# Optimization experiments

Measured on AMD Instinct MI355X. Metric: run time of the kernel, lower is better.

The kernel has to match this reference:

```python
import jax, jax.numpy as jnp
import numpy as np
import math

B, L, D, H = 2, 2048, 1024, 16
DK = D // H


def setup_inputs() -> dict:
    key = jax.random.key(0)
    ks = jax.random.split(key, 11)
    s = 1.0 / math.sqrt(D)
    inp = {
        "query": jax.random.normal(ks[0], (B, L, D), jnp.float32),
        "key": jax.random.normal(ks[1], (B, L, D), jnp.float32),
        "value": jax.random.normal(ks[2], (B, L, D), jnp.float32),
        # mask == True (==1) means masked-out; causal mask over future positions
        "mask": jnp.triu(jnp.ones((L, L), dtype=bool), k=1),
        "Wq": jax.random.normal(ks[3], (D, D), jnp.float32) * s,
        "bq": jnp.zeros((D,), jnp.float32),
        "Wk": jax.random.normal(ks[4], (D, D), jnp.float32) * s,
        "bk": jnp.zeros((D,), jnp.float32),
        "Wv": jax.random.normal(ks[5], (D, D), jnp.float32) * s,
        "bv": jnp.zeros((D,), jnp.float32),
        "Wo": jax.random.normal(ks[6], (D, D), jnp.float32) * s,
        "bo": jnp.zeros((D,), jnp.float32),
    }
    return inp


def reference(query, key, value, mask, Wq, bq, Wk, bk, Wv, bv, Wo, bo):
    # Linear projections, then split heads: [B, L, D] -> [B, H, L, DK]
    def proj(x, W, b):
        return (x @ W.T + b).reshape(B, -1, H, DK).transpose(0, 2, 1, 3)

    Q = proj(query, Wq, bq)
    K = proj(key, Wk, bk)
    V = proj(value, Wv, bv)

    scale = 1.0 / math.sqrt(DK)
    scores = jnp.einsum("bhqd,bhkd->bhqk", Q, K) * scale  # [B,H,Lq,Lk]
    scores = jnp.where(mask, -jnp.inf, scores)
    attn = jax.nn.softmax(scores, axis=-1)  # dropout p=0 (eval mode)
    out = jnp.einsum("bhqk,bhkd->bhqd", attn, V)
    out = out.transpose(0, 2, 1, 3).reshape(B, -1, D)  # merge heads
    return out @ Wo.T + bo
```

## Files before the change

### kernel.cpp

```cpp
#include <hip/hip_runtime.h>
#include <hip/hip_bf16.h>
#include <math.h>

#define NL 2048
#define ND 1024

typedef __attribute__((ext_vector_type(8))) __bf16 bf16x8;
typedef __attribute__((ext_vector_type(4))) float f32x4;
typedef __attribute__((ext_vector_type(16))) float f32x16;
typedef __attribute__((ext_vector_type(4))) short short4v;
typedef __attribute__((ext_vector_type(2))) unsigned uint2v;
typedef __attribute__((ext_vector_type(4))) unsigned uint4v;

__device__ __forceinline__ short f2bf(float f) {
    union { float f; unsigned u; } v; v.f = f;
    unsigned u = v.u;
    u += 0x7FFF + ((u >> 16) & 1);
    return (short)(u >> 16);
}

__device__ __forceinline__ unsigned cvtpk2(float lo, float hi) {
    unsigned r;
    asm("v_cvt_pk_bf16_f32 %0, %1, %2" : "=v"(r) : "v"(lo), "v"(hi));
    return r;
}

__device__ __forceinline__ void gload16(const short* g, short* l) {
    __builtin_amdgcn_global_load_lds(
        (const __attribute__((address_space(1))) void*)g,
        (__attribute__((address_space(3))) void*)l, 16, 0, 0);
}

__global__ __launch_bounds__(256) void cvt_f32_bf16_3(const float* __restrict__ a,
                                                      const float* __restrict__ b,
                                                      const float* __restrict__ c,
                                                      short* __restrict__ dst, int per) {
    const float* src = blockIdx.y == 0 ? a : blockIdx.y == 1 ? b : c;
    short* d = dst + (size_t)blockIdx.y * per;
    int i = (blockIdx.x * 256 + threadIdx.x) * 8;
    if (i < per) {
        f32x4 v0 = *(const f32x4*)&src[i];
        f32x4 v1 = *(const f32x4*)&src[i + 4];
        uint4v u = { cvtpk2(v0[0], v0[1]), cvtpk2(v0[2], v0[3]),
                     cvtpk2(v1[0], v1[1]), cvtpk2(v1[2], v1[3]) };
        *(uint4v*)&d[i] = u;
    }
}

__global__ __launch_bounds__(256) void gemm_qkv(
    const float* __restrict__ Xq, const float* __restrict__ Xk, const float* __restrict__ Xv,
    const short* __restrict__ Wqb, const short* __restrict__ Wkb, const short* __restrict__ Wvb,
    const float* __restrict__ bq, const float* __restrict__ bk, const float* __restrict__ bv,
    short* __restrict__ oq, short* __restrict__ ok, short* __restrict__ ov) {
    __shared__ alignas(16) short As[128 * 40];
    __shared__ alignas(16) short Bs[128 * 32];

    const int bid  = blockIdx.x;
    const int xcd  = bid & 7, slot = bid >> 3;
    const int panel = xcd * 12 + (slot >> 3);
    const int z    = panel >> 5;
    const int m0   = (panel & 31) * 128;
    const int n0   = (slot & 7) * 128;

    const float* X  = z == 0 ? Xq : z == 1 ? Xk : Xv;
    const short* Wb = z == 0 ? Wqb : z == 1 ? Wkb : Wvb;
    const float* bi = z == 0 ? bq : z == 1 ? bk : bv;
    short* outp     = z == 0 ? oq : z == 1 ? ok : ov;
    const float scl = z == 0 ? 0.125f * 1.44269504088896f : 1.0f;

    const int tid = threadIdx.x, lane = tid & 63, w = tid >> 6;
    const int wr = w >> 1, wc = w & 1, lr = lane >> 4, lc = lane & 15;

    const short* gB = &Wb[(n0 + w * 16 + (lane >> 2)) * 1024 + (lane & 3) * 8];
    short* lB0 = &Bs[w * 512];
    short* lB1 = &Bs[w * 512 + 2048];

    f32x4 acc[4][4] = {};

    for (int k0 = 0; k0 < 1024; k0 += 32) {
        gload16(gB + k0, lB0);
        gload16(gB + 64 * 1024 + k0, lB1);
        #pragma unroll
        for (int p = 0; p < 4; ++p) {
            int lin = p * 256 + tid;
            int row = lin >> 3;
            int col = (lin & 7) * 4;
            f32x4 v = *(const f32x4*)&X[(m0 + row) * 1024 + k0 + col];
            uint2v uu = { cvtpk2(v[0], v[1]), cvtpk2(v[2], v[3]) };
            *(uint2v*)&As[row * 40 + col] = uu;
        }
        __syncthreads();

        bf16x8 a[4], b[4];
        #pragma unroll
        for (int mt = 0; mt < 4; ++mt)
            a[mt] = *(const bf16x8*)&As[(wr * 64 + mt * 16 + lc) * 40 + lr * 8];
        #pragma unroll
        for (int nt = 0; nt < 4; ++nt)
            b[nt] = *(const bf16x8*)&Bs[(wc * 64 + nt * 16 + lc) * 32 + lr * 8];
        #pragma unroll
        for (int mt = 0; mt < 4; ++mt)
            #pragma unroll
            for (int nt = 0; nt < 4; ++nt)
                acc[mt][nt] = __builtin_amdgcn_mfma_f32_16x16x32_bf16(
                    a[mt], b[nt], acc[mt][nt], 0, 0, 0);
        __syncthreads();
    }

    #pragma unroll
    for (int mt = 0; mt < 4; ++mt)
        #pragma unroll
        for (int nt = 0; nt < 4; ++nt)
            #pragma unroll
            for (int r = 0; r < 4; ++r) {
                int grow = m0 + wr * 64 + mt * 16 + lr * 4 + r;
                int gcol = n0 + wc * 64 + nt * 16 + lc;
                float val = (acc[mt][nt][r] + bi[gcol]) * scl;
                int bh = (grow >> 11) * 16 + (gcol >> 6);
                int q  = grow & 2047;
                int dk = gcol & 63;
                size_t addr;
                if (z == 2)
                    addr = (size_t)bh * 131072 + (size_t)(q >> 6) * 4096 +
                           ((q >> 4) & 3) * 1024 + (dk >> 5) * 512 +
                           ((q >> 3) & 1) * 256 + (dk & 31) * 8 + (q & 7);
                else
                    addr = (size_t)bh * 131072 + (size_t)(q >> 5) * 2048 +
                           (dk >> 4) * 512 + ((dk >> 3) & 1) * 256 +
                           (q & 31) * 8 + (dk & 7);
                outp[addr] = f2bf(val);
            }
}

__global__ __launch_bounds__(256) void gemm_out(const short* __restrict__ Abf,
                                                const short* __restrict__ Wob,
                                                const float* __restrict__ bo,
                                                float* __restrict__ out) {
    __shared__ alignas(16) short As[128 * 32];
    __shared__ alignas(16) short Bs[128 * 32];

    const int bid = blockIdx.x;
    const int xcd = bid & 7, slot = bid >> 3;
    const int m0  = (xcd * 4 + (slot >> 3)) * 128;
    const int n0  = (slot & 7) * 128;

    const int tid = threadIdx.x, lane = tid & 63, w = tid >> 6;
    const int wr = w >> 1, wc = w & 1, lr = lane >> 4, lc = lane & 15;

    const short* gA = &Abf[(m0 + w * 16 + (lane >> 2)) * 1024 + (lane & 3) * 8];
    const short* gB = &Wob[(n0 + w * 16 + (lane >> 2)) * 1024 + (lane & 3) * 8];
    short* lA0 = &As[w * 512];
    short* lA1 = &As[w * 512 + 2048];
    short* lB0 = &Bs[w * 512];
    short* lB1 = &Bs[w * 512 + 2048];

    f32x4 acc[4][4] = {};

    for (int k0 = 0; k0 < 1024; k0 += 32) {
        gload16(gA + k0, lA0);
        gload16(gA + 64 * 1024 + k0, lA1);
        gload16(gB + k0, lB0);
        gload16(gB + 64 * 1024 + k0, lB1);
        __syncthreads();

        bf16x8 a[4], b[4];
        #pragma unroll
        for (int mt = 0; mt < 4; ++mt)
            a[mt] = *(const bf16x8*)&As[(wr * 64 + mt * 16 + lc) * 32 + lr * 8];
        #pragma unroll
        for (int nt = 0; nt < 4; ++nt)
            b[nt] = *(const bf16x8*)&Bs[(wc * 64 + nt * 16 + lc) * 32 + lr * 8];
        #pragma unroll
        for (int mt = 0; mt < 4; ++mt)
            #pragma unroll
            for (int nt = 0; nt < 4; ++nt)
                acc[mt][nt] = __builtin_amdgcn_mfma_f32_16x16x32_bf16(
                    a[mt], b[nt], acc[mt][nt], 0, 0, 0);
        __syncthreads();
    }

    #pragma unroll
    for (int mt = 0; mt < 4; ++mt)
        #pragma unroll
        for (int nt = 0; nt < 4; ++nt)
            #pragma unroll
            for (int r = 0; r < 4; ++r) {
                int grow = m0 + wr * 64 + mt * 16 + lr * 4 + r;
                int gcol = n0 + wc * 64 + nt * 16 + lc;
                out[grow * 1024 + gcol] = acc[mt][nt][r] + bo[gcol];
            }
}

__global__ __launch_bounds__(128, 3) void flash_attn(const short* __restrict__ Q,
                                                     const short* __restrict__ K,
                                                     const short* __restrict__ Vt,
                                                     short* __restrict__ AO) {
    __shared__ float mrg[64][49];

    const int tid  = threadIdx.x;
    const int lane = tid & 63;
    const int w    = tid >> 6;
    const int ql   = lane & 31;
    const int hi   = lane >> 5;

    const int bid  = blockIdx.x;
    const int xcd  = bid & 7;
    const int idx  = bid >> 3;
    const int bh   = xcd * 4 + (idx & 3);
    const int t    = 63 - (idx >> 2);
    const int q0   = t * 32;
    const int qa   = q0 + ql;
    const int nkb  = (t >> 1) + 1;
    const int nkb2 = nkb >> 1;
    const int kb_lo = w == 0 ? 0 : nkb2;
    const int kb_hi = w == 0 ? nkb2 : nkb;

    const short* Qp = Q  + (size_t)bh * 131072 + (size_t)t * 2048 + lane * 8;
    const short* Kp = K  + (size_t)bh * 131072 + lane * 8;
    const short* Vp = Vt + (size_t)bh * 131072 + lane * 8;

    bf16x8 qf[4];
    #pragma unroll
    for (int ks = 0; ks < 4; ++ks)
        qf[ks] = *(const bf16x8*)&Qp[ks * 512];

    f32x16 ot0 = {}, ot1 = {}, lacc = {};

    for (int kb = kb_lo; kb < kb_hi; ++kb) {
        bf16x8 kf[8];
        #pragma unroll
        for (int ks = 0; ks < 4; ++ks) {
            kf[2 * ks]     = *(const bf16x8*)&Kp[(size_t)(2 * kb) * 2048 + ks * 512];
            kf[2 * ks + 1] = *(const bf16x8*)&Kp[(size_t)(2 * kb + 1) * 2048 + ks * 512];
        }

        f32x16 st0 = {}, st1 = {};
        __builtin_amdgcn_s_setprio(1);
        #pragma unroll
        for (int ks = 0; ks < 4; ++ks) {
            st0 = __builtin_amdgcn_mfma_f32_32x32x16_bf16(kf[2 * ks],     qf[ks], st0, 0, 0, 0);
            st1 = __builtin_amdgcn_mfma_f32_32x32x16_bf16(kf[2 * ks + 1], qf[ks], st1, 0, 0, 0);
        }
        __builtin_amdgcn_s_setprio(0);

        bf16x8 vf[8];
        #pragma unroll
        for (int ks = 0; ks < 4; ++ks) {
            vf[2 * ks]     = *(const bf16x8*)&Vp[(size_t)kb * 4096 + ks * 1024];
            vf[2 * ks + 1] = *(const bf16x8*)&Vp[(size_t)kb * 4096 + ks * 1024 + 512];
        }

        if (kb == nkb - 1) {
            const int kv0 = kb * 64;
            #pragma unroll
            for (int r = 0; r < 16; ++r) {
                const int cr = (r & 3) + 8 * (r >> 2) + 4 * hi;
                if (kv0 + cr > qa)      st0[r] = -3.0e38f;
                if (kv0 + 32 + cr > qa) st1[r] = -3.0e38f;
            }
        }

        #pragma unroll
        for (int r = 0; r < 16; ++r) {
            st0[r] = exp2f(st0[r]);
            st1[r] = exp2f(st1[r]);
            lacc[r] += st0[r] + st1[r];
        }

        bf16x8 pf[4];
        #pragma unroll
        for (int blk = 0; blk < 2; ++blk) {
            const f32x16 s = blk ? st1 : st0;
            #pragma unroll
            for (int pks = 0; pks < 2; ++pks) {
                const int b = pks * 8;
                unsigned xa = cvtpk2(s[b + 0], s[b + 1]);
                unsigned xb = cvtpk2(s[b + 2], s[b + 3]);
                unsigned ya = cvtpk2(s[b + 4], s[b + 5]);
                unsigned yb = cvtpk2(s[b + 6], s[b + 7]);
                uint2v s0 = __builtin_amdgcn_permlane32_swap(xa, ya, false, false);
                uint2v s1 = __builtin_amdgcn_permlane32_swap(xb, yb, false, false);
                union { unsigned u[4]; bf16x8 v; } pu;
                pu.u[0] = s0[0]; pu.u[1] = s1[0]; pu.u[2] = s0[1]; pu.u[3] = s1[1];
                pf[blk * 2 + pks] = pu.v;
            }
        }

        __builtin_amdgcn_s_setprio(1);
        #pragma unroll
        for (int ks = 0; ks < 4; ++ks) {
            ot0 = __builtin_amdgcn_mfma_f32_32x32x16_bf16(vf[2 * ks],     pf[ks], ot0, 0, 0, 0);
            ot1 = __builtin_amdgcn_mfma_f32_32x32x16_bf16(vf[2 * ks + 1], pf[ks], ot1, 0, 0, 0);
        }
        __builtin_amdgcn_s_setprio(0);
    }

    if (w == 0) {
        #pragma unroll
        for (int r = 0; r < 16; ++r) {
            mrg[lane][r]      = ot0[r];
            mrg[lane][16 + r] = ot1[r];
            mrg[lane][32 + r] = lacc[r];
        }
    }
    __syncthreads();
    if (w == 1) {
        #pragma unroll
        for (int r = 0; r < 16; ++r) {
            ot0[r]  += mrg[lane][r];
            ot1[r]  += mrg[lane][16 + r];
            lacc[r] += mrg[lane][32 + r];
        }
        float sm[16];
        #pragma unroll
        for (int r = 0; r < 16; ++r) sm[r] = lacc[r];
        #pragma unroll
        for (int s = 8; s > 0; s >>= 1)
            #pragma unroll
            for (int i = 0; i < s; ++i) sm[i] += sm[i + s];
        const float l = sm[0] + __shfl_xor(sm[0], 32);
        const float inv = 1.f / l;

        const int b_ = bh >> 4, h_ = bh & 15;
        short* aoRow = AO + ((size_t)(b_ * NL + qa)) * ND + h_ * 64;
        #pragma unroll
        for (int db = 0; db < 2; ++db) {
            const f32x16 o = db ? ot1 : ot0;
            #pragma unroll
            for (int g = 0; g < 4; ++g) {
                short4v sv;
                #pragma unroll
                for (int i = 0; i < 4; ++i) sv[i] = f2bf(o[g * 4 + i] * inv);
                *(short4v*)&aoRow[db * 32 + g * 8 + 4 * hi] = sv;
            }
        }
    }
}

extern "C" void kernel_launch(void* const* d_in, const int* in_sizes, int n_in,
                              void* d_out, int out_size, void* d_ws, size_t ws_size,
                              hipStream_t stream) {
    const float* query = (const float*)d_in[0];
    const float* key   = (const float*)d_in[1];
    const float* value = (const float*)d_in[2];
    const float* Wq = (const float*)d_in[4];
    const float* bq = (const float*)d_in[5];
    const float* Wk = (const float*)d_in[6];
    const float* bk = (const float*)d_in[7];
    const float* Wv = (const float*)d_in[8];
    const float* bv = (const float*)d_in[9];
    const float* Wo = (const float*)d_in[10];
    const float* bo = (const float*)d_in[11];

    short* ws    = (short*)d_ws;
    short* q_ws  = ws;
    short* k_ws  = ws + (4 << 20);
    short* vt_ws = ws + (8 << 20);
    short* wbf   = ws + (12 << 20);
    short* ao_ws = ws + (12 << 20);
    short* wobf  = ws;

    cvt_f32_bf16_3<<<dim3(512, 3), 256, 0, stream>>>(Wq, Wk, Wv, wbf, 1 << 20);
    gemm_qkv<<<dim3(768), 256, 0, stream>>>(
        query, key, value,
        wbf, wbf + (1 << 20), wbf + (2 << 20),
        bq, bk, bv, q_ws, k_ws, vt_ws);
    flash_attn<<<dim3(2048), dim3(128), 0, stream>>>(q_ws, k_ws, vt_ws, ao_ws);
    cvt_f32_bf16_3<<<dim3(512, 1), 256, 0, stream>>>(Wo, Wo, Wo, wobf, 1 << 20);
    gemm_out<<<dim3(256), 256, 0, stream>>>(ao_ws, wobf, bo, (float*)d_out);
}
```

Measured before the change: 115.3 us.

## Double-buffer LDS tiles in QKV and output projection GEMMs

```diff
diff --git a/kernel.cpp b/kernel.cpp
--- a/kernel.cpp
+++ b/kernel.cpp
@@ -52,8 +52,8 @@
     const short* __restrict__ Wqb, const short* __restrict__ Wkb, const short* __restrict__ Wvb,
     const float* __restrict__ bq, const float* __restrict__ bk, const float* __restrict__ bv,
     short* __restrict__ oq, short* __restrict__ ok, short* __restrict__ ov) {
-    __shared__ alignas(16) short As[128 * 40];
-    __shared__ alignas(16) short Bs[128 * 32];
+    __shared__ alignas(16) short As[2][128 * 32];
+    __shared__ alignas(16) short Bs[2][128 * 32];
 
     const int bid  = blockIdx.x;
     const int xcd  = bid & 7, slot = bid >> 3;
@@ -72,39 +72,59 @@
     const int wr = w >> 1, wc = w & 1, lr = lane >> 4, lc = lane & 15;
 
     const short* gB = &Wb[(n0 + w * 16 + (lane >> 2)) * 1024 + (lane & 3) * 8];
-    short* lB0 = &Bs[w * 512];
-    short* lB1 = &Bs[w * 512 + 2048];
+    const float* gA = &X[(m0 + (tid >> 3)) * 1024 + (tid & 7) * 4];
+    const int arow = tid >> 3, acol = (tid & 7) * 4;
 
     f32x4 acc[4][4] = {};
-
-    for (int k0 = 0; k0 < 1024; k0 += 32) {
-        gload16(gB + k0, lB0);
-        gload16(gB + 64 * 1024 + k0, lB1);
-        #pragma unroll
-        for (int p = 0; p < 4; ++p) {
-            int lin = p * 256 + tid;
-            int row = lin >> 3;
-            int col = (lin & 7) * 4;
-            f32x4 v = *(const f32x4*)&X[(m0 + row) * 1024 + k0 + col];
-            uint2v uu = { cvtpk2(v[0], v[1]), cvtpk2(v[2], v[3]) };
-            *(uint2v*)&As[row * 40 + col] = uu;
-        }
-        __syncthreads();
+    f32x4 av[4];
+
+    #pragma unroll
+    for (int p = 0; p < 4; ++p) av[p] = *(const f32x4*)&gA[p * 32 * 1024];
+    gload16(gB, &Bs[0][w * 512]);
+    gload16(gB + 64 * 1024, &Bs[0][w * 512 + 2048]);
+    #pragma unroll
+    for (int p = 0; p < 4; ++p) {
+        uint2v uu = { cvtpk2(av[p][0], av[p][1]), cvtpk2(av[p][2], av[p][3]) };
+        *(uint2v*)&As[0][(p * 32 + arow) * 32 + acol] = uu;
+    }
+    __syncthreads();
+
+    int cur = 0;
+    for (int t = 0; t < 32; ++t) {
+        const int k1 = (t + 1) * 32;
+        if (t < 31) {
+            #pragma unroll
+            for (int p = 0; p < 4; ++p)
+                av[p] = *(const f32x4*)&gA[p * 32 * 1024 + k1];
+            gload16(gB + k1, &Bs[cur ^ 1][w * 512]);
+            gload16(gB + 64 * 1024 + k1, &Bs[cur ^ 1][w * 512 + 2048]);
+        }
 
         bf16x8 a[4], b[4];
         #pragma unroll
         for (int mt = 0; mt < 4; ++mt)
-            a[mt] = *(const bf16x8*)&As[(wr * 64 + mt * 16 + lc) * 40 + lr * 8];
+            a[mt] = *(const bf16x8*)&As[cur][(wr * 64 + mt * 16 + lc) * 32 + lr * 8];
         #pragma unroll
         for (int nt = 0; nt < 4; ++nt)
-            b[nt] = *(const bf16x8*)&Bs[(wc * 64 + nt * 16 + lc) * 32 + lr * 8];
+            b[nt] = *(const bf16x8*)&Bs[cur][(wc * 64 + nt * 16 + lc) * 32 + lr * 8];
+        __builtin_amdgcn_s_setprio(1);
         #pragma unroll
         for (int mt = 0; mt < 4; ++mt)
             #pragma unroll
             for (int nt = 0; nt < 4; ++nt)
                 acc[mt][nt] = __builtin_amdgcn_mfma_f32_16x16x32_bf16(
                     a[mt], b[nt], acc[mt][nt], 0, 0, 0);
+        __builtin_amdgcn_s_setprio(0);
+
+        if (t < 31) {
+            #pragma unroll
+            for (int p = 0; p < 4; ++p) {
+                uint2v uu = { cvtpk2(av[p][0], av[p][1]), cvtpk2(av[p][2], av[p][3]) };
+                *(uint2v*)&As[cur ^ 1][(p * 32 + arow) * 32 + acol] = uu;
+            }
+        }
         __syncthreads();
+        cur ^= 1;
     }
 
     #pragma unroll
@@ -136,8 +156,8 @@
                                                 const short* __restrict__ Wob,
                                                 const float* __restrict__ bo,
                                                 float* __restrict__ out) {
-    __shared__ alignas(16) short As[128 * 32];
-    __shared__ alignas(16) short Bs[128 * 32];
+    __shared__ alignas(16) short As[2][128 * 32];
+    __shared__ alignas(16) short Bs[2][128 * 32];
 
     const int bid = blockIdx.x;
     const int xcd = bid & 7, slot = bid >> 3;
@@ -149,34 +169,42 @@
 
     const short* gA = &Abf[(m0 + w * 16 + (lane >> 2)) * 1024 + (lane & 3) * 8];
     const short* gB = &Wob[(n0 + w * 16 + (lane >> 2)) * 1024 + (lane & 3) * 8];
-    short* lA0 = &As[w * 512];
-    short* lA1 = &As[w * 512 + 2048];
-    short* lB0 = &Bs[w * 512];
-    short* lB1 = &Bs[w * 512 + 2048];
 
     f32x4 acc[4][4] = {};
 
-    for (int k0 = 0; k0 < 1024; k0 += 32) {
-        gload16(gA + k0, lA0);
-        gload16(gA + 64 * 1024 + k0, lA1);
-        gload16(gB + k0, lB0);
-        gload16(gB + 64 * 1024 + k0, lB1);
-        __syncthreads();
+    gload16(gA, &As[0][w * 512]);
+    gload16(gA + 64 * 1024, &As[0][w * 512 + 2048]);
+    gload16(gB, &Bs[0][w * 512]);
+    gload16(gB + 64 * 1024, &Bs[0][w * 512 + 2048]);
+    __syncthreads();
+
+    int cur = 0;
+    for (int t = 0; t < 32; ++t) {
+        const int k1 = (t + 1) * 32;
+        if (t < 31) {
+            gload16(gA + k1, &As[cur ^ 1][w * 512]);
+            gload16(gA + 64 * 1024 + k1, &As[cur ^ 1][w * 512 + 2048]);
+            gload16(gB + k1, &Bs[cur ^ 1][w * 512]);
+            gload16(gB + 64 * 1024 + k1, &Bs[cur ^ 1][w * 512 + 2048]);
+        }
 
         bf16x8 a[4], b[4];
         #pragma unroll
         for (int mt = 0; mt < 4; ++mt)
-            a[mt] = *(const bf16x8*)&As[(wr * 64 + mt * 16 + lc) * 32 + lr * 8];
+            a[mt] = *(const bf16x8*)&As[cur][(wr * 64 + mt * 16 + lc) * 32 + lr * 8];
         #pragma unroll
         for (int nt = 0; nt < 4; ++nt)
-            b[nt] = *(const bf16x8*)&Bs[(wc * 64 + nt * 16 + lc) * 32 + lr * 8];
+            b[nt] = *(const bf16x8*)&Bs[cur][(wc * 64 + nt * 16 + lc) * 32 + lr * 8];
+        __builtin_amdgcn_s_setprio(1);
         #pragma unroll
         for (int mt = 0; mt < 4; ++mt)
             #pragma unroll
             for (int nt = 0; nt < 4; ++nt)
                 acc[mt][nt] = __builtin_amdgcn_mfma_f32_16x16x32_bf16(
                     a[mt], b[nt], acc[mt][nt], 0, 0, 0);
+        __builtin_amdgcn_s_setprio(0);
         __syncthreads();
+        cur ^= 1;
     }
 
     #pragma unroll
```

Result: slower. 119.6 us, median of 2 (+3.8%).

## Pre-convert activations to bf16 and use 4-stage async-LDS pipelined GEMM core

Applied to the files above, without the earlier changes.

```diff
diff --git a/kernel.cpp b/kernel.cpp
--- a/kernel.cpp
+++ b/kernel.cpp
@@ -31,12 +31,14 @@
         (__attribute__((address_space(3))) void*)l, 16, 0, 0);
 }
 
-__global__ __launch_bounds__(256) void cvt_f32_bf16_3(const float* __restrict__ a,
-                                                      const float* __restrict__ b,
-                                                      const float* __restrict__ c,
-                                                      short* __restrict__ dst, int per) {
+__global__ __launch_bounds__(256) void cvt3(const float* __restrict__ a,
+                                            const float* __restrict__ b,
+                                            const float* __restrict__ c,
+                                            short* __restrict__ da,
+                                            short* __restrict__ db,
+                                            short* __restrict__ dc, int per) {
     const float* src = blockIdx.y == 0 ? a : blockIdx.y == 1 ? b : c;
-    short* d = dst + (size_t)blockIdx.y * per;
+    short* d = blockIdx.y == 0 ? da : blockIdx.y == 1 ? db : dc;
     int i = (blockIdx.x * 256 + threadIdx.x) * 8;
     if (i < per) {
         f32x4 v0 = *(const f32x4*)&src[i];
@@ -47,65 +49,98 @@
     }
 }
 
-__global__ __launch_bounds__(256) void gemm_qkv(
-    const float* __restrict__ Xq, const float* __restrict__ Xk, const float* __restrict__ Xv,
-    const short* __restrict__ Wqb, const short* __restrict__ Wkb, const short* __restrict__ Wvb,
-    const float* __restrict__ bq, const float* __restrict__ bk, const float* __restrict__ bv,
-    short* __restrict__ oq, short* __restrict__ ok, short* __restrict__ ov) {
-    __shared__ alignas(16) short As[128 * 40];
-    __shared__ alignas(16) short Bs[128 * 32];
-
-    const int bid  = blockIdx.x;
-    const int xcd  = bid & 7, slot = bid >> 3;
-    const int panel = xcd * 12 + (slot >> 3);
-    const int z    = panel >> 5;
-    const int m0   = (panel & 31) * 128;
-    const int n0   = (slot & 7) * 128;
-
-    const float* X  = z == 0 ? Xq : z == 1 ? Xk : Xv;
-    const short* Wb = z == 0 ? Wqb : z == 1 ? Wkb : Wvb;
-    const float* bi = z == 0 ? bq : z == 1 ? bk : bv;
-    short* outp     = z == 0 ? oq : z == 1 ? ok : ov;
-    const float scl = z == 0 ? 0.125f * 1.44269504088896f : 1.0f;
-
-    const int tid = threadIdx.x, lane = tid & 63, w = tid >> 6;
-    const int wr = w >> 1, wc = w & 1, lr = lane >> 4, lc = lane & 15;
-
-    const short* gB = &Wb[(n0 + w * 16 + (lane >> 2)) * 1024 + (lane & 3) * 8];
-    short* lB0 = &Bs[w * 512];
-    short* lB1 = &Bs[w * 512 + 2048];
-
-    f32x4 acc[4][4] = {};
-
-    for (int k0 = 0; k0 < 1024; k0 += 32) {
-        gload16(gB + k0, lB0);
-        gload16(gB + 64 * 1024 + k0, lB1);
-        #pragma unroll
-        for (int p = 0; p < 4; ++p) {
-            int lin = p * 256 + tid;
-            int row = lin >> 3;
-            int col = (lin & 7) * 4;
-            f32x4 v = *(const f32x4*)&X[(m0 + row) * 1024 + k0 + col];
-            uint2v uu = { cvtpk2(v[0], v[1]), cvtpk2(v[2], v[3]) };
-            *(uint2v*)&As[row * 40 + col] = uu;
-        }
-        __syncthreads();
+__device__ __forceinline__ void gemm_core(const short* gA, const short* gB,
+                                          short (*As)[4096], short (*Bs)[4096],
+                                          int w, int wr, int wc, int lr, int lc,
+                                          f32x4 acc[4][4]) {
+    gload16(gA,         &As[0][w * 512]);
+    gload16(gA + 65536, &As[0][w * 512 + 2048]);
+    gload16(gB,         &Bs[0][w * 512]);
+    gload16(gB + 65536, &Bs[0][w * 512 + 2048]);
+    gload16(gA + 32,         &As[1][w * 512]);
+    gload16(gA + 65536 + 32, &As[1][w * 512 + 2048]);
+    gload16(gB + 32,         &Bs[1][w * 512]);
+    gload16(gB + 65536 + 32, &Bs[1][w * 512 + 2048]);
+
+    for (int t = 0; t < 30; ++t) {
+        const int ws_ = (t + 2) & 3, rd = t & 3;
+        const int k2 = (t + 2) * 32;
+        gload16(gA + k2,         &As[ws_][w * 512]);
+        gload16(gA + 65536 + k2, &As[ws_][w * 512 + 2048]);
+        gload16(gB + k2,         &Bs[ws_][w * 512]);
+        gload16(gB + 65536 + k2, &Bs[ws_][w * 512 + 2048]);
+        asm volatile("s_waitcnt vmcnt(8)" ::: "memory");
+        __builtin_amdgcn_s_barrier();
+        asm volatile("" ::: "memory");
 
         bf16x8 a[4], b[4];
         #pragma unroll
         for (int mt = 0; mt < 4; ++mt)
-            a[mt] = *(const bf16x8*)&As[(wr * 64 + mt * 16 + lc) * 40 + lr * 8];
+            a[mt] = *(const bf16x8*)&As[rd][(wr * 64 + mt * 16 + lc) * 32 + lr * 8];
         #pragma unroll
         for (int nt = 0; nt < 4; ++nt)
-            b[nt] = *(const bf16x8*)&Bs[(wc * 64 + nt * 16 + lc) * 32 + lr * 8];
+            b[nt] = *(const bf16x8*)&Bs[rd][(wc * 64 + nt * 16 + lc) * 32 + lr * 8];
+        __builtin_amdgcn_s_setprio(1);
         #pragma unroll
         for (int mt = 0; mt < 4; ++mt)
             #pragma unroll
             for (int nt = 0; nt < 4; ++nt)
                 acc[mt][nt] = __builtin_amdgcn_mfma_f32_16x16x32_bf16(
                     a[mt], b[nt], acc[mt][nt], 0, 0, 0);
-        __syncthreads();
-    }
+        __builtin_amdgcn_s_setprio(0);
+    }
+    #pragma unroll
+    for (int pt = 0; pt < 2; ++pt) {
+        if (pt == 0) asm volatile("s_waitcnt vmcnt(4)" ::: "memory");
+        else         asm volatile("s_waitcnt vmcnt(0)" ::: "memory");
+        __builtin_amdgcn_s_barrier();
+        asm volatile("" ::: "memory");
+        const int rd = 2 + pt;
+        bf16x8 a[4], b[4];
+        #pragma unroll
+        for (int mt = 0; mt < 4; ++mt)
+            a[mt] = *(const bf16x8*)&As[rd][(wr * 64 + mt * 16 + lc) * 32 + lr * 8];
+        #pragma unroll
+        for (int nt = 0; nt < 4; ++nt)
+            b[nt] = *(const bf16x8*)&Bs[rd][(wc * 64 + nt * 16 + lc) * 32 + lr * 8];
+        #pragma unroll
+        for (int mt = 0; mt < 4; ++mt)
+            #pragma unroll
+            for (int nt = 0; nt < 4; ++nt)
+                acc[mt][nt] = __builtin_amdgcn_mfma_f32_16x16x32_bf16(
+                    a[mt], b[nt], acc[mt][nt], 0, 0, 0);
+    }
+}
+
+__global__ __launch_bounds__(256) void gemm_qk(
+    const short* __restrict__ Xqb, const short* __restrict__ Xkb,
+    const short* __restrict__ Wqb, const short* __restrict__ Wkb,
+    const float* __restrict__ bq, const float* __restrict__ bk,
+    short* __restrict__ oq, short* __restrict__ ok) {
+    __shared__ alignas(16) short As[4][4096];
+    __shared__ alignas(16) short Bs[4][4096];
+
+    const int bid  = blockIdx.x;
+    const int xcd  = bid & 7, slot = bid >> 3;
+    const int panel = xcd * 8 + (slot >> 3);
+    const int zz   = panel >> 5;
+    const int m0   = (panel & 31) * 128;
+    const int n0   = (slot & 7) * 128;
+
+    const short* Ab = zz ? Xkb : Xqb;
+    const short* Wb = zz ? Wkb : Wqb;
+    const float* bi = zz ? bk : bq;
+    short* outp     = zz ? ok : oq;
+    const float scl = zz ? 1.0f : 0.125f * 1.44269504088896f;
+
+    const int tid = threadIdx.x, lane = tid & 63, w = tid >> 6;
+    const int wr = w >> 1, wc = w & 1, lr = lane >> 4, lc = lane & 15;
+
+    const short* gA = &Ab[(m0 + w * 16 + (lane >> 2)) * 1024 + (lane & 3) * 8];
+    const short* gB = &Wb[(n0 + w * 16 + (lane >> 2)) * 1024 + (lane & 3) * 8];
+
+    f32x4 acc[4][4] = {};
+    gemm_core(gA, gB, As, Bs, w, wr, wc, lr, lc, acc);
 
     #pragma unroll
     for (int mt = 0; mt < 4; ++mt)
@@ -119,16 +154,50 @@
                 int bh = (grow >> 11) * 16 + (gcol >> 6);
                 int q  = grow & 2047;
                 int dk = gcol & 63;
-                size_t addr;
-                if (z == 2)
-                    addr = (size_t)bh * 131072 + (size_t)(q >> 6) * 4096 +
-                           ((q >> 4) & 3) * 1024 + (dk >> 5) * 512 +
-                           ((q >> 3) & 1) * 256 + (dk & 31) * 8 + (q & 7);
-                else
-                    addr = (size_t)bh * 131072 + (size_t)(q >> 5) * 2048 +
-                           (dk >> 4) * 512 + ((dk >> 3) & 1) * 256 +
-                           (q & 31) * 8 + (dk & 7);
+                size_t addr = (size_t)bh * 131072 + (size_t)(q >> 5) * 2048 +
+                              (dk >> 4) * 512 + ((dk >> 3) & 1) * 256 +
+                              (q & 31) * 8 + (dk & 7);
                 outp[addr] = f2bf(val);
+            }
+}
+
+__global__ __launch_bounds__(256) void gemm_v(
+    const short* __restrict__ Xvb, const short* __restrict__ Wvb,
+    const float* __restrict__ bv, short* __restrict__ ov) {
+    __shared__ alignas(16) short As[4][4096];
+    __shared__ alignas(16) short Bs[4][4096];
+
+    const int bid = blockIdx.x;
+    const int xcd = bid & 7, slot = bid >> 3;
+    const int m0  = (xcd * 4 + (slot >> 3)) * 128;
+    const int n0  = (slot & 7) * 128;
+
+    const int tid = threadIdx.x, lane = tid & 63, w = tid >> 6;
+    const int wr = w >> 1, wc = w & 1, lr = lane >> 4, lc = lane & 15;
+
+    const short* gA = &Xvb[(m0 + w * 16 + (lane >> 2)) * 1024 + (lane & 3) * 8];
+    const short* gB = &Wvb[(n0 + w * 16 + (lane >> 2)) * 1024 + (lane & 3) * 8];
+
+    f32x4 acc[4][4] = {};
+    gemm_core(gA, gB, As, Bs, w, wr, wc, lr, lc, acc);
+
+    #pragma unroll
+    for (int mt = 0; mt < 4; ++mt)
+        #pragma unroll
+        for (int nt = 0; nt < 4; ++nt)
+            #pragma unroll
+            for (int r = 0; r < 4; ++r) {
+                int grow = m0 + wr * 64 + mt * 16 + lr * 4 + r;
+                int gcol = n0 + wc * 64 + nt * 16 + lc;
+                float val = acc[mt][nt][r] + bv[gcol];
+                int bh = (grow >> 11) * 16 + (gcol >> 6);
+                int q  = grow & 2047;
+                int dk = gcol & 63;
+                size_t addr = (size_t)bh * 131072 + (size_t)(q >> 6) * 4096 +
+                              ((q >> 4) & 3) * 1024 + (dk >> 5) * 512 +
+                              ((q >> 3) & 1) * 256 + (dk & 31) * 8 + (q & 7);
+                outp_store: outp_store_dummy:;
+                ov[addr] = f2bf(val);
             }
 }
 
@@ -136,8 +205,8 @@
                                                 const short* __restrict__ Wob,
                                                 const float* __restrict__ bo,
                                                 float* __restrict__ out) {
-    __shared__ alignas(16) short As[128 * 32];
-    __shared__ alignas(16) short Bs[128 * 32];
+    __shared__ alignas(16) short As[4][4096];
+    __shared__ alignas(16) short Bs[4][4096];
 
     const int bid = blockIdx.x;
     const int xcd = bid & 7, slot = bid >> 3;
@@ -149,35 +218,9 @@
 
     const short* gA = &Abf[(m0 + w * 16 + (lane >> 2)) * 1024 + (lane & 3) * 8];
     const short* gB = &Wob[(n0 + w * 16 + (lane >> 2)) * 1024 + (lane & 3) * 8];
-    short* lA0 = &As[w * 512];
-    short* lA1 = &As[w * 512 + 2048];
-    short* lB0 = &Bs[w * 512];
-    short* lB1 = &Bs[w * 512 + 2048];
 
     f32x4 acc[4][4] = {};
-
-    for (int k0 = 0; k0 < 1024; k0 += 32) {
-        gload16(gA + k0, lA0);
-        gload16(gA + 64 * 1024 + k0, lA1);
-        gload16(gB + k0, lB0);
-        gload16(gB + 64 * 1024 + k0, lB1);
-        __syncthreads();
-
-        bf16x8 a[4], b[4];
-        #pragma unroll
-        for (int mt = 0; mt < 4; ++mt)
-            a[mt] = *(const bf16x8*)&As[(wr * 64 + mt * 16 + lc) * 32 + lr * 8];
-        #pragma unroll
-        for (int nt = 0; nt < 4; ++nt)
-            b[nt] = *(const bf16x8*)&Bs[(wc * 64 + nt * 16 + lc) * 32 + lr * 8];
-        #pragma unroll
-        for (int mt = 0; mt < 4; ++mt)
-            #pragma unroll
-            for (int nt = 0; nt < 4; ++nt)
-                acc[mt][nt] = __builtin_amdgcn_mfma_f32_16x16x32_bf16(
-                    a[mt], b[nt], acc[mt][nt], 0, 0, 0);
-        __syncthreads();
-    }
+    gemm_core(gA, gB, As, Bs, w, wr, wc, lr, lc, acc);
 
     #pragma unroll
     for (int mt = 0; mt < 4; ++mt)
@@ -353,19 +396,24 @@
     const float* bo = (const float*)d_in[11];
 
     short* ws    = (short*)d_ws;
+    short* dob   = (short*)d_out;
     short* q_ws  = ws;
     short* k_ws  = ws + (4 << 20);
+    short* xq    = ws + (8 << 20);
     short* vt_ws = ws + (8 << 20);
     short* wbf   = ws + (12 << 20);
     short* ao_ws = ws + (12 << 20);
     short* wobf  = ws;
-
-    cvt_f32_bf16_3<<<dim3(512, 3), 256, 0, stream>>>(Wq, Wk, Wv, wbf, 1 << 20);
-    gemm_qkv<<<dim3(768), 256, 0, stream>>>(
-        query, key, value,
-        wbf, wbf + (1 << 20), wbf + (2 << 20),
-        bq, bk, bv, q_ws, k_ws, vt_ws);
+    short* xk    = dob;
+    short* xv    = dob + (4 << 20);
+
+    cvt3<<<dim3(512, 3), 256, 0, stream>>>(Wq, Wk, Wv,
+                                           wbf, wbf + (1 << 20), wbf + (2 << 20), 1 << 20);
+    cvt3<<<dim3(2048, 3), 256, 0, stream>>>(query, key, value, xq, xk, xv, 4 << 20);
+    gemm_qk<<<dim3(512), 256, 0, stream>>>(xq, xk, wbf, wbf + (1 << 20),
+                                           bq, bk, q_ws, k_ws);
+    gemm_v<<<dim3(256), 256, 0, stream>>>(xv, wbf + (2 << 20), bv, vt_ws);
     flash_attn<<<dim3(2048), dim3(128), 0, stream>>>(q_ws, k_ws, vt_ws, ao_ws);
-    cvt_f32_bf16_3<<<dim3(512, 1), 256, 0, stream>>>(Wo, Wo, Wo, wobf, 1 << 20);
+    cvt3<<<dim3(512, 1), 256, 0, stream>>>(Wo, Wo, Wo, wobf, wobf, wobf, 1 << 20);
     gemm_out<<<dim3(256), 256, 0, stream>>>(ao_ws, wobf, bo, (float*)d_out);
 }
```

Result: slower. 133.8 us (+16.1%).
